# Kernel optimization log

Measured on AMD Instinct MI355X. Metric: run time of the kernel, lower is better.

## Reference

```python
import jax, jax.numpy as jnp
import numpy as np

NEG_INF = -1.0e9  # matches torch masked_fill value


def setup_inputs() -> dict:
    key = jax.random.key(0)
    k1, k2 = jax.random.split(key)
    bs, seq_len, emb_dim = 8, 4096, 512
    max_num_patches = 1024
    h = jax.random.normal(k1, (bs, seq_len, emb_dim), dtype=jnp.float32)
    patch_ids = jnp.sort(
        jax.random.randint(k2, (bs, seq_len), 0, max_num_patches), axis=-1
    )
    return {"h": h, "patch_ids": patch_ids,
            "max_num_patches": max_num_patches, "k": 2}


def reference(h, patch_ids, max_num_patches, k):
    """topk_mean pooling: for each patch (segment) and embedding dim, average
    the top-k values of h among tokens belonging to that patch. Patches with
    fewer than k tokens average only the available tokens; empty patches -> 0.
    Faithful to the torch scatter_reduce(amax)+mask loop."""
    bs, seq_len, emb_dim = h.shape
    b_idx = jnp.arange(bs)[:, None]  # [bs,1] broadcast with patch_ids [bs,seq]
    # tokens-per-patch counts (equivalent of one_hot.sum(dim=1))
    counts = jnp.zeros((bs, max_num_patches), h.dtype).at[b_idx, patch_ids].add(1.0)

    h_work = h
    collected = []
    for _ in range(k):  # k is a small static constant (default 2)
        # segmented amax over tokens -> [bs, P, E]; empty patches get 0
        # (torch scatter_reduce with include_self=False on a zeros base)
        scattered = (jnp.full((bs, max_num_patches, emb_dim), -jnp.inf, h.dtype)
                     .at[b_idx, patch_ids].max(h_work))
        current_max = jnp.where(counts[:, :, None] > 0, scattered, jnp.zeros((), h.dtype))
        collected.append(current_max)
        # gather per-token patch max and mask out positions equal to it
        cur_exp = current_max[b_idx, patch_ids]  # [bs, seq, E]
        h_work = jnp.where(h_work == cur_exp, jnp.asarray(NEG_INF, h.dtype), h_work)

    topk_vals = jnp.stack(collected, axis=2)  # [bs, P, k, E]
    valid = (jnp.arange(k)[None, None, :] < counts[:, :, None]).astype(h.dtype)  # [bs,P,k]
    sum_valid = (topk_vals * valid[..., None]).sum(axis=2)          # [bs, P, E]
    num_valid = jnp.clip(valid.sum(axis=2), 1.0, None)              # [bs, P]
    return sum_valid / num_valid[..., None]
```

## Files before the change

### kernel.cpp

```cpp
#include <hip/hip_runtime.h>


#define NEG_INF (-1.0e9f)
#define D 8

__global__ __launch_bounds__(256) void seg_bounds_scatter(
    const int* __restrict__ pid,
    const int* __restrict__ d_P,
    int*       __restrict__ bnd,
    int bs_seq, int pairs)
{
    const int P   = *d_P;
    const int bs  = pairs / P;
    const int seq = bs_seq / bs;

    const int idx = blockIdx.x * blockDim.x + threadIdx.x;
    if (idx >= bs_seq) return;
    const int b = idx / seq;
    const int t = idx - b * seq;

    const int* row  = pid + (size_t)b * seq;
    int*       brow = bnd + (size_t)b * P;
    const int  cur  = row[t];

    if (t == 0) {
        for (int p = 0; p <= cur; ++p) brow[p] = 0;
    } else {
        const int prev = row[t - 1];
        for (int p = prev + 1; p <= cur; ++p) brow[p] = t;
    }
    if (t == seq - 1) {
        for (int p = cur + 1; p < P; ++p) brow[p] = seq;
    }
}

__global__ __launch_bounds__(128) void topk_mean_pool(
    const float* __restrict__ h,
    const int*   __restrict__ bnd,
    const int*   __restrict__ d_P,
    const int*   __restrict__ d_k,
    float*       __restrict__ out,
    int bs_seq, int pairs, int E)
{
    const int P   = *d_P;
    const int bs  = pairs / P;
    const int seq = bs_seq / bs;
    const int kk  = *d_k;

    const int pair = blockIdx.x;
    const int b    = pair / P;
    const int p    = pair - b * P;

    const int start = bnd[pair];
    const int end   = (p == P - 1) ? seq : bnd[pair + 1];
    const int n     = end - start;

    const int Ed4 = E >> 2;
    const float4* hb   = (const float4*)h + (size_t)b * seq * Ed4;
    float4*       out4 = (float4*)out + (size_t)pair * Ed4;

    for (int c = threadIdx.x; c < Ed4; c += blockDim.x) {
        float4 r;
        if (n == 0) {
            r = make_float4(0.f, 0.f, 0.f, 0.f);
        } else {
            float4 m1 = make_float4(-INFINITY, -INFINITY, -INFINITY, -INFINITY);
            float4 m2 = m1;
            int t = start;
            while (t < end) {
                const int nload = min(D, end - t);
                float4 v[D];
#pragma unroll
                for (int d = 0; d < D; ++d)
                    if (d < nload) v[d] = hb[(size_t)(t + d) * Ed4 + c];
#pragma unroll
                for (int d = 0; d < D; ++d) {
                    if (d < nload) {
                        const float4 vv = v[d];
                        if (vv.x > m1.x) { m2.x = m1.x; m1.x = vv.x; }
                        else if (vv.x < m1.x && vv.x > m2.x) { m2.x = vv.x; }
                        if (vv.y > m1.y) { m2.y = m1.y; m1.y = vv.y; }
                        else if (vv.y < m1.y && vv.y > m2.y) { m2.y = vv.y; }
                        if (vv.z > m1.z) { m2.z = m1.z; m1.z = vv.z; }
                        else if (vv.z < m1.z && vv.z > m2.z) { m2.z = vv.z; }
                        if (vv.w > m1.w) { m2.w = m1.w; m1.w = vv.w; }
                        else if (vv.w < m1.w && vv.w > m2.w) { m2.w = vv.w; }
                    }
                }
                t += nload;
            }
            if (n == 1 || kk == 1) {
                r = m1;
            } else {
                r.x = 0.5f * (m1.x + fmaxf(m2.x, NEG_INF));
                r.y = 0.5f * (m1.y + fmaxf(m2.y, NEG_INF));
                r.z = 0.5f * (m1.z + fmaxf(m2.z, NEG_INF));
                r.w = 0.5f * (m1.w + fmaxf(m2.w, NEG_INF));
            }
        }
        out4[c] = r;
    }
}

extern "C" void kernel_launch(void* const* d_in, const int* in_sizes, int n_in,
                              void* d_out, int out_size, void* d_ws, size_t ws_size,
                              hipStream_t stream) {
    const float* h   = (const float*)d_in[0];
    const int*   pid = (const int*)d_in[1];
    const int*   d_P = (const int*)d_in[2];
    const int*   d_k = (const int*)d_in[3];
    float*       out = (float*)d_out;
    int*         bnd = (int*)d_ws;
    (void)n_in; (void)ws_size;

    const int h_elems = in_sizes[0];
    const int bs_seq  = in_sizes[1];
    const int E       = h_elems / bs_seq;
    const int pairs   = out_size / E;

    {
        dim3 grid((bs_seq + 255) / 256), block(256);
        seg_bounds_scatter<<<grid, block, 0, stream>>>(pid, d_P, bnd,
                                                       bs_seq, pairs);
    }
    {
        dim3 grid(pairs), block(128);
        topk_mean_pool<<<grid, block, 0, stream>>>(h, bnd, d_P, d_k, out,
                                                   bs_seq, pairs, E);
    }
}
```

Baseline: 106.9 us.

## Fuse segment-boundary computation into pooling kernel via per-block binary search

Removes the separate boundary-scatter kernel and workspace. Each pooling block now binary-searches the sorted patch ids to find its own segment start and end. The loads of h and the output stores switch to nontemporal builtins so streaming data bypasses cache retention. This saves one kernel launch and a global round trip, at the cost of a short serial binary search plus a block barrier at the start of every block.

```diff
diff --git a/kernel.cpp b/kernel.cpp
--- a/kernel.cpp
+++ b/kernel.cpp
@@ -4,39 +4,11 @@
 #define NEG_INF (-1.0e9f)
 #define D 8
 
-__global__ __launch_bounds__(256) void seg_bounds_scatter(
-    const int* __restrict__ pid,
-    const int* __restrict__ d_P,
-    int*       __restrict__ bnd,
-    int bs_seq, int pairs)
-{
-    const int P   = *d_P;
-    const int bs  = pairs / P;
-    const int seq = bs_seq / bs;
+typedef float vf4 __attribute__((ext_vector_type(4)));
 
-    const int idx = blockIdx.x * blockDim.x + threadIdx.x;
-    if (idx >= bs_seq) return;
-    const int b = idx / seq;
-    const int t = idx - b * seq;
-
-    const int* row  = pid + (size_t)b * seq;
-    int*       brow = bnd + (size_t)b * P;
-    const int  cur  = row[t];
-
-    if (t == 0) {
-        for (int p = 0; p <= cur; ++p) brow[p] = 0;
-    } else {
-        const int prev = row[t - 1];
-        for (int p = prev + 1; p <= cur; ++p) brow[p] = t;
-    }
-    if (t == seq - 1) {
-        for (int p = cur + 1; p < P; ++p) brow[p] = seq;
-    }
-}
-
-__global__ __launch_bounds__(128) void topk_mean_pool(
+__global__ __launch_bounds__(128) void topk_mean_pool_fused(
     const float* __restrict__ h,
-    const int*   __restrict__ bnd,
+    const int*   __restrict__ pid,
     const int*   __restrict__ d_P,
     const int*   __restrict__ d_k,
     float*       __restrict__ out,
@@ -51,32 +23,47 @@
     const int b    = pair / P;
     const int p    = pair - b * P;
 
-    const int start = bnd[pair];
-    const int end   = (p == P - 1) ? seq : bnd[pair + 1];
+    __shared__ int sb[2];
+    if (threadIdx.x < 2) {
+        const int  tgt = p + (int)threadIdx.x;
+        const int* row = pid + (size_t)b * seq;
+        int lo = 0, hi = seq;
+        while (lo < hi) {
+            const int mid = (lo + hi) >> 1;
+            if (row[mid] < tgt) lo = mid + 1; else hi = mid;
+        }
+        sb[threadIdx.x] = lo;
+    }
+    __syncthreads();
+
+    const int start = sb[0];
+    const int end   = sb[1];
     const int n     = end - start;
 
     const int Ed4 = E >> 2;
-    const float4* hb   = (const float4*)h + (size_t)b * seq * Ed4;
-    float4*       out4 = (float4*)out + (size_t)pair * Ed4;
+    const vf4* hb   = reinterpret_cast<const vf4*>(h) + (size_t)b * seq * Ed4;
+    vf4*       out4 = reinterpret_cast<vf4*>(out) + (size_t)pair * Ed4;
 
     for (int c = threadIdx.x; c < Ed4; c += blockDim.x) {
-        float4 r;
+        vf4 r;
         if (n == 0) {
-            r = make_float4(0.f, 0.f, 0.f, 0.f);
+            r = (vf4){0.f, 0.f, 0.f, 0.f};
         } else {
-            float4 m1 = make_float4(-INFINITY, -INFINITY, -INFINITY, -INFINITY);
-            float4 m2 = m1;
+            vf4 m1 = (vf4){-INFINITY, -INFINITY, -INFINITY, -INFINITY};
+            vf4 m2 = m1;
             int t = start;
             while (t < end) {
                 const int nload = min(D, end - t);
-                float4 v[D];
+                vf4 v[D];
 #pragma unroll
                 for (int d = 0; d < D; ++d)
-                    if (d < nload) v[d] = hb[(size_t)(t + d) * Ed4 + c];
+                    if (d < nload)
+                        v[d] = __builtin_nontemporal_load(
+                                   &hb[(size_t)(t + d) * Ed4 + c]);
 #pragma unroll
                 for (int d = 0; d < D; ++d) {
                     if (d < nload) {
-                        const float4 vv = v[d];
+                        const vf4 vv = v[d];
                         if (vv.x > m1.x) { m2.x = m1.x; m1.x = vv.x; }
                         else if (vv.x < m1.x && vv.x > m2.x) { m2.x = vv.x; }
                         if (vv.y > m1.y) { m2.y = m1.y; m1.y = vv.y; }
@@ -98,7 +85,7 @@
                 r.w = 0.5f * (m1.w + fmaxf(m2.w, NEG_INF));
             }
         }
-        out4[c] = r;
+        __builtin_nontemporal_store(r, &out4[c]);
     }
 }
 
@@ -110,22 +97,14 @@
     const int*   d_P = (const int*)d_in[2];
     const int*   d_k = (const int*)d_in[3];
     float*       out = (float*)d_out;
-    int*         bnd = (int*)d_ws;
-    (void)n_in; (void)ws_size;
+    (void)d_ws; (void)ws_size; (void)n_in;
 
     const int h_elems = in_sizes[0];
     const int bs_seq  = in_sizes[1];
     const int E       = h_elems / bs_seq;
     const int pairs   = out_size / E;
 
-    {
-        dim3 grid((bs_seq + 255) / 256), block(256);
-        seg_bounds_scatter<<<grid, block, 0, stream>>>(pid, d_P, bnd,
-                                                       bs_seq, pairs);
-    }
-    {
-        dim3 grid(pairs), block(128);
-        topk_mean_pool<<<grid, block, 0, stream>>>(h, bnd, d_P, d_k, out,
-                                                   bs_seq, pairs, E);
-    }
+    dim3 grid(pairs), block(128);
+    topk_mean_pool_fused<<<grid, block, 0, stream>>>(h, pid, d_P, d_k, out,
+                                                     bs_seq, pairs, E);
 }
```

New measurement: 118.9 us. 11.3% more time.
